# Optimization experiments

Hardware: AMD Instinct MI355X
Metric: run time of the kernel (lower is better)

The kernel has to match this reference:

```python
import jax, jax.numpy as jnp
import numpy as np
from jax.scipy.special import i0

# --- module constants (from Transform.__init__) ---
H = 320          # image size per dim
OS = 2           # grid oversampling ratio
G = H * OS       # oversampled grid size (640)
W = 6            # Kaiser-Bessel kernel width (torchkbnufft default numpoints)
BETA = float(np.pi * np.sqrt((W / OS) ** 2 * (OS - 0.5) ** 2 - 0.8))  # Beatty beta
S_FULL = 800     # spokes in full trajectory
R = H * OS       # readout points per spoke (640)
B, C = 8, 1      # slices, coils


def _golden_traj(n_spokes, n_read):
    """Golden-angle radial trajectory; k radius = H/2 = 160 (matches traj/160*pi scaling)."""
    ga = np.pi * 2.0 / (1.0 + np.sqrt(5.0))  # ~111.246 degrees
    ang = np.arange(n_spokes) * ga
    r = np.linspace(-H / 2, H / 2, n_read, endpoint=False)
    kx = (r[None, :] * np.cos(ang)[:, None]).astype(np.float32)
    ky = (r[None, :] * np.sin(ang)[:, None]).astype(np.float32)
    return kx, ky


def _kb(d):
    """Kaiser-Bessel kernel, d in oversampled-grid units, support |d|<=W/2."""
    arg = jnp.clip(1.0 - (2.0 * d / W) ** 2, 0.0, None)
    return i0(BETA * jnp.sqrt(arg)) / i0(jnp.float32(BETA))


def _apod1d(n):
    """Analytic Fourier transform of the KB kernel -> image-domain apodization."""
    f = (jnp.arange(n, dtype=jnp.float32) - n / 2) / G  # cycles per grid sample
    t = BETA ** 2 - (jnp.pi * W * f) ** 2
    z = jnp.maximum(jnp.sqrt(jnp.abs(t)), 1e-7)
    a = jnp.where(t > 0, jnp.sinh(z), jnp.sin(z)) / z
    return a / a[n // 2]  # normalize center to 1


def _ktoi(k):
    """Centered inverse 2D FFT (k-space -> image)."""
    return jnp.fft.fftshift(
        jnp.fft.ifft2(jnp.fft.ifftshift(k, axes=(-2, -1)), axes=(-2, -1), norm='ortho'),
        axes=(-2, -1))


def _mean_std_norm_complex(x):
    ax = (-3, -2, -1)
    def n(v):
        m = v.mean(axis=ax, keepdims=True)
        s = v.std(axis=ax, keepdims=True, ddof=1)  # torch std default: unbiased
        return (v - m) / s
    return n(x.real) + 1j * n(x.imag)


def _nufft(image, traj_kx, traj_ky):
    """Type-2 KB NUFFT: image (B,C,H,H) complex -> k samples (B,C,S,R)."""
    S, Rr = traj_kx.shape
    # apodization correction then oversampled centered FFT
    ap = _apod1d(H)
    x = image / (ap[:, None] * ap[None, :])
    xp = jnp.zeros(image.shape[:-2] + (G, G), jnp.complex64)
    xp = xp.at[..., H // 2:H // 2 + H, H // 2:H // 2 + H].set(x)
    Xos = jnp.fft.fft2(jnp.fft.ifftshift(xp, axes=(-2, -1)), axes=(-2, -1))
    # non-uniform grid coords: omega = traj/160*pi -> g = omega*G/(2pi) = traj*G/H
    gx = (traj_kx * (G / H)).reshape(-1)  # (P,)
    gy = (traj_ky * (G / H)).reshape(-1)
    ix0 = jnp.floor(gx).astype(jnp.int32) - W // 2 + 1
    iy0 = jnp.floor(gy).astype(jnp.int32) - W // 2 + 1
    out = jnp.zeros(image.shape[:-2] + (gx.shape[0],), jnp.complex64)
    for jx in range(W):  # fixed 6x6 neighbor taps
        ixu = ix0 + jx
        wx = _kb(gx - ixu)
        ix = jnp.mod(ixu, G)
        for jy in range(W):
            iyu = iy0 + jy
            w = (wx * _kb(gy - iyu)).astype(jnp.complex64)
            iy = jnp.mod(iyu, G)
            out = out + w * Xos[..., ix, iy]
    return out.reshape(image.shape[:-2] + (S, Rr))


def setup_inputs() -> dict:
    key = jax.random.key(0)
    k1, k2 = jax.random.split(key)
    kspace_r = jax.random.normal(k1, (B, C, H, H), jnp.float32)
    kspace_i = jax.random.normal(k2, (B, C, H, H), jnp.float32)
    tkx, tky = _golden_traj(S_FULL, R)
    return {'kspace_r': kspace_r, 'kspace_i': kspace_i,
            'traj_kx': jnp.asarray(tkx), 'traj_ky': jnp.asarray(tky)}


def reference(kspace_r, kspace_i, traj_kx, traj_ky):
    kspace = (kspace_r + 1j * kspace_i).astype(jnp.complex64)
    image = _mean_std_norm_complex(_ktoi(kspace))
    kspace_full = _nufft(image, traj_kx, traj_ky)
    return kspace_full
```

## Files before the change

kernel.cpp:

```cpp
#include <hip/hip_runtime.h>
#include <math.h>

#ifndef M_PI
#define M_PI 3.14159265358979323846
#endif

#define HH   320
#define GG   640
#define NB   8
#define PTS  512000

typedef __attribute__((ext_vector_type(8))) short short8_t;
typedef __attribute__((ext_vector_type(4))) float f32x4;

__device__ __forceinline__ float bessel_i0f(float x){
  if (x < 3.75f){
    float t = (x*x) * (1.0f/(3.75f*3.75f));
    return 1.0f + t*(3.5156229f + t*(3.0899424f + t*(1.2067492f +
                 t*(0.2659732f + t*(0.0360768f + t*0.0045813f)))));
  } else {
    float t = 3.75f/x;
    float p = 0.39894228f + t*(0.01328592f + t*(0.00225319f + t*(-0.00157565f +
              t*(0.00916281f + t*(-0.02057706f + t*(0.02635537f +
              t*(-0.01647633f + t*0.00392377f)))))));
    return expf(x)*rsqrtf(x)*p;
  }
}

__device__ __forceinline__ float kbw(float d, float beta, float inv_i0b){
  float q = d * 0.33333333333333f;
  float u = 1.0f - q*q;
  u = fmaxf(u, 0.0f);
  return bessel_i0f(beta * sqrtf(u)) * inv_i0b;
}

__device__ __forceinline__ short bfr(float x){
  unsigned u = __float_as_uint(x);
  u = (u + 0x7fffu + ((u>>16)&1u)) >> 16;
  return (short)u;
}
__device__ __forceinline__ unsigned pkbf(float2 v){
  unsigned a = __float_as_uint(v.x);
  a = (a + 0x7fffu + ((a>>16)&1u)) >> 16;
  unsigned b = __float_as_uint(v.y);
  b = (b + 0x7fffu + ((b>>16)&1u)) & 0xffff0000u;
  return a | b;
}

__global__ void build_m1bf(short* __restrict__ M1r, short* __restrict__ M1i){
  int idx = blockIdx.x*256 + threadIdx.x;
  if (idx >= HH*HH) return;
  int x = idx / HH, k = idx - x*HH;
  int r = (x*k) % HH;
  float ang = (float)r * (6.283185307179586f/(float)HH);
  float s, c; sincosf(ang, &s, &c);
  float sg = ((x + k) & 1) ? -0.05590169943749474f : 0.05590169943749474f;
  M1r[idx] = bfr(sg*c);
  M1i[idx] = bfr(sg*s);
}

__global__ void build_w2(short* __restrict__ Wr, short* __restrict__ Wi){
  int idx = blockIdx.x*256 + threadIdx.x;
  if (idx >= GG*HH) return;
  int k = idx / HH, m = idx - k*HH;
  int t = (k * (m - 160)) % GG; if (t < 0) t += GG;
  float ang = (float)t * (6.283185307179586f/(float)GG);
  float s, c; sincosf(ang, &s, &c);
  Wr[idx] = bfr(c);
  Wi[idx] = bfr(-s);
}

__global__ void build_rap(float* __restrict__ rap, float beta){
  int n = threadIdx.x;
  if (n >= HH) return;
  float f = (float)(n - 160) * (1.0f/(float)GG);
  float w = 3.14159265358979f * 6.0f * f;
  float t = beta*beta - w*w;
  float z = fmaxf(sqrtf(fabsf(t)), 1e-7f);
  float a = (t > 0.0f ? sinhf(z) : sinf(z)) / z;
  float a0 = sinhf(beta) / beta;
  rap[n] = a0 / a;
}

__global__ void pack_bf(const float* __restrict__ re, const float* __restrict__ im,
                        short* __restrict__ Kr, short* __restrict__ Ki, int n){
  int i = blockIdx.x*256 + threadIdx.x;
  if (i < n){ Kr[i] = bfr(re[i]); Ki[i] = bfr(im[i]); }
}

__global__ __launch_bounds__(512)
void gemm1_mfma(const short* __restrict__ M1r, const short* __restrict__ M1i,
                const short* __restrict__ Kr,  const short* __restrict__ Ki,
                short* __restrict__ Ttr, short* __restrict__ Tti)
{
  int nwg = gridDim.x, orig = blockIdx.x;
  int qn = nwg>>3, rn = nwg&7;
  int xcd = orig&7, pos = orig>>3;
  int wg = (xcd<rn ? xcd*(qn+1) : rn*(qn+1)+(xcd-rn)*qn) + pos;
  int ti = wg % 20, tj = wg / 20;
  int i0 = ti*16, j0 = tj*16;
  int l = threadIdx.x & 63, wid = threadIdx.x >> 6;

  long aoff = (long)(j0 + (l&15))*HH + ((l>>4)<<3);
  const short* pmr = M1r + aoff;
  const short* pmi = M1i + aoff;
  long boff = (long)wid*102400 + (long)(i0 + (l&15))*HH + ((l>>4)<<3);
  const short* pkr = Kr + boff;
  const short* pki = Ki + boff;

  f32x4 accRa = {0.f,0.f,0.f,0.f}, accRb = {0.f,0.f,0.f,0.f}, accI = {0.f,0.f,0.f,0.f};
  #pragma unroll
  for (int kt = 0; kt < 320; kt += 32){
    short8_t mR = *(const short8_t*)(pmr + kt);
    short8_t mI = *(const short8_t*)(pmi + kt);
    short8_t kR = *(const short8_t*)(pkr + kt);
    short8_t kI = *(const short8_t*)(pki + kt);
    accRa = __builtin_amdgcn_mfma_f32_16x16x32_bf16(mR, kR, accRa, 0,0,0);
    accRb = __builtin_amdgcn_mfma_f32_16x16x32_bf16(mI, kI, accRb, 0,0,0);
    accI  = __builtin_amdgcn_mfma_f32_16x16x32_bf16(mR, kI, accI, 0,0,0);
    accI  = __builtin_amdgcn_mfma_f32_16x16x32_bf16(mI, kR, accI, 0,0,0);
  }
  int col = l & 15, r0 = (l>>4)*4;
  #pragma unroll
  for (int r=0;r<4;r++){
    long o = (long)wid*102400 + (long)(j0+r0+r)*HH + i0+col;
    Ttr[o] = bfr(accRa[r] - accRb[r]);
    Tti[o] = bfr(accI[r]);
  }
}

__global__ __launch_bounds__(512)
void gemm2_mfma(const short* __restrict__ M1r, const short* __restrict__ M1i,
                const short* __restrict__ Ttr, const short* __restrict__ Tti,
                float2* __restrict__ P)
{
  int nwg = gridDim.x, orig = blockIdx.x;
  int qn = nwg>>3, rn = nwg&7;
  int xcd = orig&7, pos = orig>>3;
  int wg = (xcd<rn ? xcd*(qn+1) : rn*(qn+1)+(xcd-rn)*qn) + pos;
  int tj = wg % 20, ti = wg / 20;
  int i0 = ti*16, j0 = tj*16;
  int l = threadIdx.x & 63, wid = threadIdx.x >> 6;

  long aoff = (long)(i0 + (l&15))*HH + ((l>>4)<<3);
  const short* pmr = M1r + aoff;
  const short* pmi = M1i + aoff;
  long boff = (long)wid*102400 + (long)(j0 + (l&15))*HH + ((l>>4)<<3);
  const short* ptr = Ttr + boff;
  const short* pti = Tti + boff;

  f32x4 accRa = {0.f,0.f,0.f,0.f}, accRb = {0.f,0.f,0.f,0.f}, accI = {0.f,0.f,0.f,0.f};
  #pragma unroll
  for (int kt = 0; kt < 320; kt += 32){
    short8_t mR = *(const short8_t*)(pmr + kt);
    short8_t mI = *(const short8_t*)(pmi + kt);
    short8_t tR = *(const short8_t*)(ptr + kt);
    short8_t tI = *(const short8_t*)(pti + kt);
    accRa = __builtin_amdgcn_mfma_f32_16x16x32_bf16(mR, tR, accRa, 0,0,0);
    accRb = __builtin_amdgcn_mfma_f32_16x16x32_bf16(mI, tI, accRb, 0,0,0);
    accI  = __builtin_amdgcn_mfma_f32_16x16x32_bf16(mR, tI, accI, 0,0,0);
    accI  = __builtin_amdgcn_mfma_f32_16x16x32_bf16(mI, tR, accI, 0,0,0);
  }
  int col = l & 15, r0 = (l>>4)*4;
  #pragma unroll
  for (int r=0;r<4;r++){
    long o = (long)wid*102400 + (long)(i0+r0+r)*HH + j0+col;
    P[o] = make_float2(accRa[r] - accRb[r], accI[r]);
  }
}

__global__ void stats_part(const float2* __restrict__ img, double* __restrict__ part){
  int slice = blockIdx.y, seg = blockIdx.x;
  const float2* p = img + (long)slice*(HH*HH) + (long)seg*3200;
  double sr=0.0, si=0.0, srr=0.0, sii=0.0;
  for (int i = threadIdx.x; i < 3200; i += 256){
    float2 v = p[i];
    sr += (double)v.x; si += (double)v.y;
    srr += (double)v.x*(double)v.x; sii += (double)v.y*(double)v.y;
  }
  __shared__ double sh[256];
  double vals[4] = {sr, si, srr, sii};
  #pragma unroll
  for (int q=0;q<4;q++){
    sh[threadIdx.x] = vals[q];
    __syncthreads();
    for (int s=128; s>0; s>>=1){
      if (threadIdx.x < s) sh[threadIdx.x] += sh[threadIdx.x + s];
      __syncthreads();
    }
    if (threadIdx.x == 0) part[((long)slice*32 + seg)*4 + q] = sh[0];
    __syncthreads();
  }
}

__global__ void stats_fin(const double* __restrict__ part, float4* __restrict__ stats){
  int b = blockIdx.x;
  int t = threadIdx.x;
  __shared__ double sh[64];
  double red[4];
  #pragma unroll
  for (int q=0;q<4;q++){
    sh[t] = (t < 32) ? part[((long)b*32 + t)*4 + q] : 0.0;
    __syncthreads();
    for (int s=32; s>0; s>>=1){
      if (t < s) sh[t] += sh[t + s];
      __syncthreads();
    }
    red[q] = sh[0];
    __syncthreads();
  }
  if (t == 0){
    double N = (double)(HH*HH);
    double mr = red[0]/N, mi = red[1]/N;
    double vr = (red[2] - N*mr*mr)/(N-1.0);
    double vi = (red[3] - N*mi*mi)/(N-1.0);
    stats[b] = make_float4((float)mr, (float)mi,
                           (float)(1.0/sqrt(vr)), (float)(1.0/sqrt(vi)));
  }
}

__global__ __launch_bounds__(256)
void tnorm(const float2* __restrict__ img, const float4* __restrict__ stats,
           const float* __restrict__ rap,
           short* __restrict__ xnTr, short* __restrict__ xnTi){
  __shared__ float2 tile[32][33];
  int b = blockIdx.z;
  int i0 = blockIdx.y*32, j0 = blockIdx.x*32;
  int tx = threadIdx.x & 31, ty = threadIdx.x >> 5;
  float4 st = stats[b];
  #pragma unroll
  for (int r=0;r<4;r++){
    int i = i0 + ty + r*8, j = j0 + tx;
    float2 v = img[(long)b*102400 + (long)i*HH + j];
    float sc = rap[i]*rap[j];
    tile[ty+r*8][tx] = make_float2((v.x-st.x)*st.z*sc, (v.y-st.y)*st.w*sc);
  }
  __syncthreads();
  #pragma unroll
  for (int r=0;r<4;r++){
    int j = j0 + ty + r*8, i = i0 + tx;
    float2 v = tile[tx][ty+r*8];
    long o = (long)b*102400 + (long)j*HH + i;
    xnTr[o] = bfr(v.x);
    xnTi[o] = bfr(v.y);
  }
}

template<int NC>
__global__ __launch_bounds__(64*NC)
void cgemm3_mfma(const short* __restrict__ Wr, const short* __restrict__ Wi,
                 const short* __restrict__ xnTr, const short* __restrict__ xnTi,
                 short* __restrict__ Ur, short* __restrict__ Ui, int slice0)
{
  int nwg = gridDim.x, orig = blockIdx.x;
  int qn = nwg>>3, rn = nwg&7;
  int xcd = orig&7, pos = orig>>3;
  int wg = (xcd<rn ? xcd*(qn+1) : rn*(qn+1)+(xcd-rn)*qn) + pos;
  int bj = wg % 20, bi = wg / 20;
  int i0 = bi*16, j0 = bj*16;
  int l = threadIdx.x & 63, wid = threadIdx.x >> 6;

  long aoff = (long)(i0 + (l&15))*HH + ((l>>4)<<3);
  const short* pwr = Wr + aoff;
  const short* pwi = Wi + aoff;
  long boff = (long)(slice0+wid)*102400 + (long)(j0 + (l&15))*HH + ((l>>4)<<3);
  const short* pxr = xnTr + boff;
  const short* pxi = xnTi + boff;

  f32x4 accRa = {0.f,0.f,0.f,0.f}, accRb = {0.f,0.f,0.f,0.f}, accI = {0.f,0.f,0.f,0.f};
  #pragma unroll
  for (int kt = 0; kt < 320; kt += 32){
    short8_t wR = *(const short8_t*)(pwr + kt);
    short8_t wI = *(const short8_t*)(pwi + kt);
    short8_t xR = *(const short8_t*)(pxr + kt);
    short8_t xI = *(const short8_t*)(pxi + kt);
    accRa = __builtin_amdgcn_mfma_f32_16x16x32_bf16(wR, xR, accRa, 0,0,0);
    accRb = __builtin_amdgcn_mfma_f32_16x16x32_bf16(wI, xI, accRb, 0,0,0);
    accI  = __builtin_amdgcn_mfma_f32_16x16x32_bf16(wR, xI, accI, 0,0,0);
    accI  = __builtin_amdgcn_mfma_f32_16x16x32_bf16(wI, xR, accI, 0,0,0);
  }
  int col = l & 15, r0 = (l>>4)*4;
  #pragma unroll
  for (int r=0;r<4;r++){
    long o = (long)wid*204800 + (long)(i0+r0+r)*HH + j0+col;
    Ur[o] = bfr(accRa[r] - accRb[r]);
    Ui[o] = bfr(accI[r]);
  }
}

template<int NC>
__global__ __launch_bounds__(64*NC)
void cgemm4_mfma(const short* __restrict__ Ur, const short* __restrict__ Ui,
                 const short* __restrict__ Wr, const short* __restrict__ Wi,
                 unsigned* __restrict__ Xos)
{
  __shared__ unsigned sh[256*NC];
  int nwg = gridDim.x, orig = blockIdx.x;
  int qn = nwg>>3, rn = nwg&7;
  int xcd = orig&7, pos = orig>>3;
  int wg = (xcd<rn ? xcd*(qn+1) : rn*(qn+1)+(xcd-rn)*qn) + pos;
  int bj = wg % 40, bi = wg / 40;
  int i0 = bi*16, j0 = bj*16;
  int l = threadIdx.x & 63, wid = threadIdx.x >> 6;

  long aoff = (long)wid*204800 + (long)(i0 + (l&15))*HH + ((l>>4)<<3);
  const short* par = Ur + aoff;
  const short* pai = Ui + aoff;
  long boff = (long)(j0 + (l&15))*HH + ((l>>4)<<3);
  const short* pbr = Wr + boff;
  const short* pbi = Wi + boff;

  f32x4 accRa = {0.f,0.f,0.f,0.f}, accRb = {0.f,0.f,0.f,0.f}, accI = {0.f,0.f,0.f,0.f};
  #pragma unroll
  for (int kt = 0; kt < 320; kt += 32){
    short8_t aR = *(const short8_t*)(par + kt);
    short8_t aI = *(const short8_t*)(pai + kt);
    short8_t bR = *(const short8_t*)(pbr + kt);
    short8_t bI = *(const short8_t*)(pbi + kt);
    accRa = __builtin_amdgcn_mfma_f32_16x16x32_bf16(aR, bR, accRa, 0,0,0);
    accRb = __builtin_amdgcn_mfma_f32_16x16x32_bf16(aI, bI, accRb, 0,0,0);
    accI  = __builtin_amdgcn_mfma_f32_16x16x32_bf16(aR, bI, accI, 0,0,0);
    accI  = __builtin_amdgcn_mfma_f32_16x16x32_bf16(aI, bR, accI, 0,0,0);
  }

  int col = l & 15, r0 = (l>>4)*4;
  #pragma unroll
  for (int r=0;r<4;r++)
    sh[(r0+r)*16*NC + col*NC + wid] = pkbf(make_float2(accRa[r]-accRb[r], accI[r]));
  __syncthreads();

  int t = threadIdx.x;
  int row = t/(4*NC), q = t - row*(4*NC);
  uint4 v = ((const uint4*)(sh + row*16*NC))[q];
  ((uint4*)(Xos + ((long)(i0+row)*GG + j0)*NC))[q] = v;
}

template<int NC>
__global__ __launch_bounds__(384)
void interp6(const float* __restrict__ tkx, const float* __restrict__ tky,
             const unsigned* __restrict__ Xos, float* __restrict__ out,
             int slice0, int cplx, float beta, float inv_i0b){
  __shared__ float2 sh[NC][6][64];
  __shared__ float swy[6][64];
  int tid = threadIdx.x;
  int ptl = tid & 63;
  int jx  = tid >> 6;
  int p   = blockIdx.x*64 + ptl;

  float gx = tkx[p]*2.0f, gy = tky[p]*2.0f;
  int ix0 = (int)floorf(gx) - 2;
  int iy0 = (int)floorf(gy) - 2;

  int ixu = ix0 + jx;
  int ixm = (ixu < 0) ? ixu + GG : ((ixu >= GG) ? ixu - GG : ixu);
  float wxj = kbw(gx - (float)ixu, beta, inv_i0b);
  swy[jx][ptl] = kbw(gy - (float)(iy0 + jx), beta, inv_i0b);

  int iym[6];
  #pragma unroll
  for (int j=0;j<6;j++){
    int iyu = iy0 + j;
    iym[j] = (iyu < 0) ? iyu + GG : ((iyu >= GG) ? iyu - GG : iyu);
  }
  __syncthreads();
  float wy[6];
  #pragma unroll
  for (int j=0;j<6;j++) wy[j] = swy[j][ptl];

  float2 acc[NC];
  #pragma unroll
  for (int s=0;s<NC;s++) acc[s] = make_float2(0.f, 0.f);

  const unsigned* rowp = Xos + (long)ixm*(GG*NC);
  #pragma unroll
  for (int jy=0;jy<6;jy++){
    float w = wy[jy];
    const unsigned* s2 = rowp + iym[jy]*NC;
    unsigned uu[NC];
    if constexpr (NC == 8){
      uint4 v0 = ((const uint4*)s2)[0], v1 = ((const uint4*)s2)[1];
      uu[0]=v0.x; uu[1]=v0.y; uu[2]=v0.z; uu[3]=v0.w;
      uu[4]=v1.x; uu[5]=v1.y; uu[6]=v1.z; uu[7]=v1.w;
    } else if constexpr (NC == 4){
      uint4 v = *(const uint4*)s2;
      uu[0]=v.x; uu[1]=v.y; uu[2]=v.z; uu[3]=v.w;
    } else if constexpr (NC == 2){
      uint2 v = *(const uint2*)s2;
      uu[0]=v.x; uu[1]=v.y;
    } else {
      uu[0] = s2[0];
    }
    #pragma unroll
    for (int s=0;s<NC;s++){
      float re = __uint_as_float(uu[s] << 16);
      float im = __uint_as_float(uu[s] & 0xffff0000u);
      acc[s].x = fmaf(w, re, acc[s].x);
      acc[s].y = fmaf(w, im, acc[s].y);
    }
  }
  #pragma unroll
  for (int s=0;s<NC;s++)
    sh[s][jx][ptl] = make_float2(acc[s].x*wxj, acc[s].y*wxj);
  __syncthreads();

  for (int t2 = tid; t2 < 64*NC; t2 += 384){
    int pt = t2 & 63;
    int s  = t2 >> 6;
    float2 r = make_float2(0.f, 0.f);
    #pragma unroll
    for (int j=0;j<6;j++){
      float2 v = sh[s][j][pt];
      r.x += v.x; r.y += v.y;
    }
    long pg = (long)blockIdx.x*64 + pt;
    if (cplx){
      ((float2*)out)[(long)(slice0+s)*PTS + pg] = r;
    } else {
      out[(long)(slice0+s)*PTS + pg] = r.x;
    }
  }
}

extern "C" void kernel_launch(void* const* d_in, const int* in_sizes, int n_in,
                              void* d_out, int out_size, void* d_ws, size_t ws_size,
                              hipStream_t stream) {
  const float* kr  = (const float*)d_in[0];
  const float* ki  = (const float*)d_in[1];
  const float* tkx = (const float*)d_in[2];
  const float* tky = (const float*)d_in[3];
  char* ws = (char*)d_ws;

  short*  M1r   = (short*)(ws + 0);
  short*  M1i   = (short*)(ws + 204800);
  short*  Wr    = (short*)(ws + 409600);
  short*  Wi    = (short*)(ws + 819200);
  float*  rap   = (float*) (ws + 1228800);
  float4* stats = (float4*)(ws + 1230080);
  double* part  = (double*)(ws + 1230208);
  short*  Kr    = (short*)(ws + 1238400);
  short*  Ki    = (short*)(ws + 2876800);
  short*  Ttr   = (short*)(ws + 4515200);
  short*  Tti   = (short*)(ws + 6153600);
  float2* P     = (float2*)(ws + 7792000);
  short*  xnTr  = (short*)(ws + 14345600);
  short*  xnTi  = (short*)(ws + 15984000);

  int nc = 1;
  if      (ws_size >= (size_t)(17622400 + 8L*1638400)) nc = 8;
  else if (ws_size >= (size_t)(17622400 + 4L*1638400)) nc = 4;
  else if (ws_size >= (size_t)(17622400 + 2L*1638400)) nc = 2;
  if (ws_size < (size_t)(17622400 + 1638400)) return;

  short*    Ur  = (short*)(ws + 7792000);
  short*    Ui  = (short*)(ws + 7792000 + (long)nc*409600);
  unsigned* Xos = (unsigned*)(ws + 17622400);

  int cplx = (out_size >= 8192000) ? 1 : 0;

  double beta_d = M_PI * sqrt(9.0*2.25 - 0.8);
  double qq = beta_d*beta_d/4.0, term = 1.0, i0b = 1.0;
  for (int k=1;k<64;k++){ term *= qq/((double)k*(double)k); i0b += term; }
  float beta = (float)beta_d;
  float inv_i0b = (float)(1.0/i0b);

  build_m1bf<<<400, 256, 0, stream>>>(M1r, M1i);
  build_w2  <<<800, 256, 0, stream>>>(Wr, Wi);
  build_rap <<<1,   320, 0, stream>>>(rap, beta);
  pack_bf   <<<3200,256, 0, stream>>>(kr, ki, Kr, Ki, NB*HH*HH);

  gemm1_mfma<<<400, 512, 0, stream>>>(M1r, M1i, Kr, Ki, Ttr, Tti);
  gemm2_mfma<<<400, 512, 0, stream>>>(M1r, M1i, Ttr, Tti, P);
  stats_part<<<dim3(32,NB), 256, 0, stream>>>(P, part);
  stats_fin <<<NB, 64, 0, stream>>>(part, stats);
  tnorm<<<dim3(10,10,NB), 256, 0, stream>>>(P, stats, rap, xnTr, xnTi);

  for (int c = 0; c < NB/nc; ++c){
    switch (nc){
      case 8:
        cgemm3_mfma<8><<<800, 512,0,stream>>>(Wr,Wi,xnTr,xnTi,Ur,Ui, c*8);
        cgemm4_mfma<8><<<1600,512,0,stream>>>(Ur,Ui,Wr,Wi,Xos);
        interp6<8><<<8000,384,0,stream>>>(tkx,tky,Xos,(float*)d_out, c*8, cplx, beta, inv_i0b);
        break;
      case 4:
        cgemm3_mfma<4><<<800, 256,0,stream>>>(Wr,Wi,xnTr,xnTi,Ur,Ui, c*4);
        cgemm4_mfma<4><<<1600,256,0,stream>>>(Ur,Ui,Wr,Wi,Xos);
        interp6<4><<<8000,384,0,stream>>>(tkx,tky,Xos,(float*)d_out, c*4, cplx, beta, inv_i0b);
        break;
      case 2:
        cgemm3_mfma<2><<<800, 128,0,stream>>>(Wr,Wi,xnTr,xnTi,Ur,Ui, c*2);
        cgemm4_mfma<2><<<1600,128,0,stream>>>(Ur,Ui,Wr,Wi,Xos);
        interp6<2><<<8000,384,0,stream>>>(tkx,tky,Xos,(float*)d_out, c*2, cplx, beta, inv_i0b);
        break;
      default:
        cgemm3_mfma<1><<<800,  64,0,stream>>>(Wr,Wi,xnTr,xnTi,Ur,Ui, c);
        cgemm4_mfma<1><<<1600, 64,0,stream>>>(Ur,Ui,Wr,Wi,Xos);
        interp6<1><<<8000,384,0,stream>>>(tkx,tky,Xos,(float*)d_out, c, cplx, beta, inv_i0b);
        break;
    }
  }
}
```

Before: 299.4 us.

## Fuse setup kernels, fold stats into gemm2, store bf16 image, use 32x32 MFMA

Merges the four setup kernels into one launch. The mean/variance statistics are now reduced inside gemm2's epilogue with wavefront shuffles, which removes the stats_part pass. The intermediate image is stored as bf16 planes instead of float2, halving that traffic. The cgemm3/cgemm4 stages switch from 16x16x32 to 32x32x16 MFMA tiles with four times fewer workgroups, trading parallelism for more reuse per instruction. The bf16 image adds rounding before normalization, and the statistics are now accumulated in float per lane before the double reduction.

```diff
diff --git a/kernel.cpp b/kernel.cpp
--- a/kernel.cpp
+++ b/kernel.cpp
@@ -10,8 +10,9 @@
 #define NB   8
 #define PTS  512000
 
-typedef __attribute__((ext_vector_type(8))) short short8_t;
-typedef __attribute__((ext_vector_type(4))) float f32x4;
+typedef __attribute__((ext_vector_type(8)))  short short8_t;
+typedef __attribute__((ext_vector_type(4)))  float f32x4;
+typedef __attribute__((ext_vector_type(16))) float f32x16;
 
 __device__ __forceinline__ float bessel_i0f(float x){
   if (x < 3.75f){
@@ -39,6 +40,9 @@
   u = (u + 0x7fffu + ((u>>16)&1u)) >> 16;
   return (short)u;
 }
+__device__ __forceinline__ float bf2f(short v){
+  return __uint_as_float(((unsigned)(unsigned short)v) << 16);
+}
 __device__ __forceinline__ unsigned pkbf(float2 v){
   unsigned a = __float_as_uint(v.x);
   a = (a + 0x7fffu + ((a>>16)&1u)) >> 16;
@@ -47,45 +51,48 @@
   return a | b;
 }
 
-__global__ void build_m1bf(short* __restrict__ M1r, short* __restrict__ M1i){
-  int idx = blockIdx.x*256 + threadIdx.x;
-  if (idx >= HH*HH) return;
-  int x = idx / HH, k = idx - x*HH;
-  int r = (x*k) % HH;
-  float ang = (float)r * (6.283185307179586f/(float)HH);
-  float s, c; sincosf(ang, &s, &c);
-  float sg = ((x + k) & 1) ? -0.05590169943749474f : 0.05590169943749474f;
-  M1r[idx] = bfr(sg*c);
-  M1i[idx] = bfr(sg*s);
-}
-
-__global__ void build_w2(short* __restrict__ Wr, short* __restrict__ Wi){
-  int idx = blockIdx.x*256 + threadIdx.x;
-  if (idx >= GG*HH) return;
-  int k = idx / HH, m = idx - k*HH;
-  int t = (k * (m - 160)) % GG; if (t < 0) t += GG;
-  float ang = (float)t * (6.283185307179586f/(float)GG);
-  float s, c; sincosf(ang, &s, &c);
-  Wr[idx] = bfr(c);
-  Wi[idx] = bfr(-s);
-}
-
-__global__ void build_rap(float* __restrict__ rap, float beta){
-  int n = threadIdx.x;
-  if (n >= HH) return;
-  float f = (float)(n - 160) * (1.0f/(float)GG);
-  float w = 3.14159265358979f * 6.0f * f;
-  float t = beta*beta - w*w;
-  float z = fmaxf(sqrtf(fabsf(t)), 1e-7f);
-  float a = (t > 0.0f ? sinhf(z) : sinf(z)) / z;
-  float a0 = sinhf(beta) / beta;
-  rap[n] = a0 / a;
-}
-
-__global__ void pack_bf(const float* __restrict__ re, const float* __restrict__ im,
-                        short* __restrict__ Kr, short* __restrict__ Ki, int n){
-  int i = blockIdx.x*256 + threadIdx.x;
-  if (i < n){ Kr[i] = bfr(re[i]); Ki[i] = bfr(im[i]); }
+__global__ void build_all(const float* __restrict__ kr, const float* __restrict__ ki,
+                          short* __restrict__ M1r, short* __restrict__ M1i,
+                          short* __restrict__ Wr,  short* __restrict__ Wi,
+                          float* __restrict__ rap,
+                          short* __restrict__ Kr,  short* __restrict__ Ki,
+                          float beta){
+  int blk = blockIdx.x, tid = threadIdx.x;
+  if (blk < 400){
+    int idx = blk*256 + tid;
+    if (idx >= HH*HH) return;
+    int x = idx / HH, k = idx - x*HH;
+    int r = (x*k) % HH;
+    float ang = (float)r * (6.283185307179586f/(float)HH);
+    float s, c; sincosf(ang, &s, &c);
+    float sg = ((x + k) & 1) ? -0.05590169943749474f : 0.05590169943749474f;
+    M1r[idx] = bfr(sg*c);
+    M1i[idx] = bfr(sg*s);
+  } else if (blk < 1200){
+    int idx = (blk-400)*256 + tid;
+    if (idx >= GG*HH) return;
+    int k = idx / HH, m = idx - k*HH;
+    int t = (k * (m - 160)) % GG; if (t < 0) t += GG;
+    float ang = (float)t * (6.283185307179586f/(float)GG);
+    float s, c; sincosf(ang, &s, &c);
+    Wr[idx] = bfr(c);
+    Wi[idx] = bfr(-s);
+  } else if (blk < 4400){
+    int idx = (blk-1200)*256 + tid;
+    if (idx >= NB*HH*HH) return;
+    Kr[idx] = bfr(kr[idx]);
+    Ki[idx] = bfr(ki[idx]);
+  } else {
+    for (int n = tid; n < HH; n += 256){
+      float f = (float)(n - 160) * (1.0f/(float)GG);
+      float w = 3.14159265358979f * 6.0f * f;
+      float t = beta*beta - w*w;
+      float z = fmaxf(sqrtf(fabsf(t)), 1e-7f);
+      float a = (t > 0.0f ? sinhf(z) : sinf(z)) / z;
+      float a0 = sinhf(beta) / beta;
+      rap[n] = a0 / a;
+    }
+  }
 }
 
 __global__ __launch_bounds__(512)
@@ -132,7 +139,8 @@
 __global__ __launch_bounds__(512)
 void gemm2_mfma(const short* __restrict__ M1r, const short* __restrict__ M1i,
                 const short* __restrict__ Ttr, const short* __restrict__ Tti,
-                float2* __restrict__ P)
+                short* __restrict__ Pr, short* __restrict__ Pi,
+                double* __restrict__ part)
 {
   int nwg = gridDim.x, orig = blockIdx.x;
   int qn = nwg>>3, rn = nwg&7;
@@ -162,47 +170,48 @@
     accI  = __builtin_amdgcn_mfma_f32_16x16x32_bf16(mI, tR, accI, 0,0,0);
   }
   int col = l & 15, r0 = (l>>4)*4;
+  float sr=0.f, si=0.f, srr=0.f, sii=0.f;
   #pragma unroll
   for (int r=0;r<4;r++){
+    float re = accRa[r] - accRb[r];
+    float im = accI[r];
     long o = (long)wid*102400 + (long)(i0+r0+r)*HH + j0+col;
-    P[o] = make_float2(accRa[r] - accRb[r], accI[r]);
-  }
-}
-
-__global__ void stats_part(const float2* __restrict__ img, double* __restrict__ part){
-  int slice = blockIdx.y, seg = blockIdx.x;
-  const float2* p = img + (long)slice*(HH*HH) + (long)seg*3200;
-  double sr=0.0, si=0.0, srr=0.0, sii=0.0;
-  for (int i = threadIdx.x; i < 3200; i += 256){
-    float2 v = p[i];
-    sr += (double)v.x; si += (double)v.y;
-    srr += (double)v.x*(double)v.x; sii += (double)v.y*(double)v.y;
-  }
-  __shared__ double sh[256];
-  double vals[4] = {sr, si, srr, sii};
-  #pragma unroll
-  for (int q=0;q<4;q++){
-    sh[threadIdx.x] = vals[q];
-    __syncthreads();
-    for (int s=128; s>0; s>>=1){
-      if (threadIdx.x < s) sh[threadIdx.x] += sh[threadIdx.x + s];
-      __syncthreads();
-    }
-    if (threadIdx.x == 0) part[((long)slice*32 + seg)*4 + q] = sh[0];
-    __syncthreads();
+    Pr[o] = bfr(re);
+    Pi[o] = bfr(im);
+    sr += re; si += im; srr += re*re; sii += im*im;
+  }
+  double d0 = sr, d1 = si, d2 = srr, d3 = sii;
+  #pragma unroll
+  for (int off = 32; off > 0; off >>= 1){
+    d0 += __shfl_down(d0, off);
+    d1 += __shfl_down(d1, off);
+    d2 += __shfl_down(d2, off);
+    d3 += __shfl_down(d3, off);
+  }
+  if (l == 0){
+    long pidx = ((long)wid*400 + wg)*4;
+    part[pidx  ] = d0;
+    part[pidx+1] = d1;
+    part[pidx+2] = d2;
+    part[pidx+3] = d3;
   }
 }
 
 __global__ void stats_fin(const double* __restrict__ part, float4* __restrict__ stats){
   int b = blockIdx.x;
   int t = threadIdx.x;
-  __shared__ double sh[64];
+  __shared__ double sh[256];
+  double loc[4] = {0.0,0.0,0.0,0.0};
+  for (int w = t; w < 400; w += 256){
+    const double* p = part + ((long)b*400 + w)*4;
+    loc[0] += p[0]; loc[1] += p[1]; loc[2] += p[2]; loc[3] += p[3];
+  }
   double red[4];
   #pragma unroll
   for (int q=0;q<4;q++){
-    sh[t] = (t < 32) ? part[((long)b*32 + t)*4 + q] : 0.0;
+    sh[t] = loc[q];
     __syncthreads();
-    for (int s=32; s>0; s>>=1){
+    for (int s=128; s>0; s>>=1){
       if (t < s) sh[t] += sh[t + s];
       __syncthreads();
     }
@@ -220,8 +229,8 @@
 }
 
 __global__ __launch_bounds__(256)
-void tnorm(const float2* __restrict__ img, const float4* __restrict__ stats,
-           const float* __restrict__ rap,
+void tnorm(const short* __restrict__ Pr, const short* __restrict__ Pi,
+           const float4* __restrict__ stats, const float* __restrict__ rap,
            short* __restrict__ xnTr, short* __restrict__ xnTi){
   __shared__ float2 tile[32][33];
   int b = blockIdx.z;
@@ -231,9 +240,10 @@
   #pragma unroll
   for (int r=0;r<4;r++){
     int i = i0 + ty + r*8, j = j0 + tx;
-    float2 v = img[(long)b*102400 + (long)i*HH + j];
+    long o = (long)b*102400 + (long)i*HH + j;
+    float re = bf2f(Pr[o]), im = bf2f(Pi[o]);
     float sc = rap[i]*rap[j];
-    tile[ty+r*8][tx] = make_float2((v.x-st.x)*st.z*sc, (v.y-st.y)*st.w*sc);
+    tile[ty+r*8][tx] = make_float2((re-st.x)*st.z*sc, (im-st.y)*st.w*sc);
   }
   __syncthreads();
   #pragma unroll
@@ -256,33 +266,34 @@
   int qn = nwg>>3, rn = nwg&7;
   int xcd = orig&7, pos = orig>>3;
   int wg = (xcd<rn ? xcd*(qn+1) : rn*(qn+1)+(xcd-rn)*qn) + pos;
-  int bj = wg % 20, bi = wg / 20;
-  int i0 = bi*16, j0 = bj*16;
+  int bj = wg % 10, bi = wg / 10;
+  int i0 = bi*32, j0 = bj*32;
   int l = threadIdx.x & 63, wid = threadIdx.x >> 6;
 
-  long aoff = (long)(i0 + (l&15))*HH + ((l>>4)<<3);
+  long aoff = (long)(i0 + (l&31))*HH + ((l>>5)<<3);
   const short* pwr = Wr + aoff;
   const short* pwi = Wi + aoff;
-  long boff = (long)(slice0+wid)*102400 + (long)(j0 + (l&15))*HH + ((l>>4)<<3);
+  long boff = (long)(slice0+wid)*102400 + (long)(j0 + (l&31))*HH + ((l>>5)<<3);
   const short* pxr = xnTr + boff;
   const short* pxi = xnTi + boff;
 
-  f32x4 accRa = {0.f,0.f,0.f,0.f}, accRb = {0.f,0.f,0.f,0.f}, accI = {0.f,0.f,0.f,0.f};
-  #pragma unroll
-  for (int kt = 0; kt < 320; kt += 32){
+  f32x16 accRa = {0.f}, accRb = {0.f}, accI = {0.f};
+  #pragma unroll
+  for (int kt = 0; kt < 320; kt += 16){
     short8_t wR = *(const short8_t*)(pwr + kt);
     short8_t wI = *(const short8_t*)(pwi + kt);
     short8_t xR = *(const short8_t*)(pxr + kt);
     short8_t xI = *(const short8_t*)(pxi + kt);
-    accRa = __builtin_amdgcn_mfma_f32_16x16x32_bf16(wR, xR, accRa, 0,0,0);
-    accRb = __builtin_amdgcn_mfma_f32_16x16x32_bf16(wI, xI, accRb, 0,0,0);
-    accI  = __builtin_amdgcn_mfma_f32_16x16x32_bf16(wR, xI, accI, 0,0,0);
-    accI  = __builtin_amdgcn_mfma_f32_16x16x32_bf16(wI, xR, accI, 0,0,0);
-  }
-  int col = l & 15, r0 = (l>>4)*4;
-  #pragma unroll
-  for (int r=0;r<4;r++){
-    long o = (long)wid*204800 + (long)(i0+r0+r)*HH + j0+col;
+    accRa = __builtin_amdgcn_mfma_f32_32x32x16_bf16(wR, xR, accRa, 0,0,0);
+    accRb = __builtin_amdgcn_mfma_f32_32x32x16_bf16(wI, xI, accRb, 0,0,0);
+    accI  = __builtin_amdgcn_mfma_f32_32x32x16_bf16(wR, xI, accI, 0,0,0);
+    accI  = __builtin_amdgcn_mfma_f32_32x32x16_bf16(wI, xR, accI, 0,0,0);
+  }
+  int col = l & 31, rhi = 4*(l>>5);
+  #pragma unroll
+  for (int r=0;r<16;r++){
+    int row = (r&3) + 8*(r>>2) + rhi;
+    long o = (long)wid*204800 + (long)(i0+row)*HH + j0+col;
     Ur[o] = bfr(accRa[r] - accRb[r]);
     Ui[o] = bfr(accI[r]);
   }
@@ -294,45 +305,52 @@
                  const short* __restrict__ Wr, const short* __restrict__ Wi,
                  unsigned* __restrict__ Xos)
 {
-  __shared__ unsigned sh[256*NC];
+  __shared__ unsigned sh[1024*NC];
   int nwg = gridDim.x, orig = blockIdx.x;
   int qn = nwg>>3, rn = nwg&7;
   int xcd = orig&7, pos = orig>>3;
   int wg = (xcd<rn ? xcd*(qn+1) : rn*(qn+1)+(xcd-rn)*qn) + pos;
-  int bj = wg % 40, bi = wg / 40;
-  int i0 = bi*16, j0 = bj*16;
+  int bj = wg % 20, bi = wg / 20;
+  int i0 = bi*32, j0 = bj*32;
   int l = threadIdx.x & 63, wid = threadIdx.x >> 6;
 
-  long aoff = (long)wid*204800 + (long)(i0 + (l&15))*HH + ((l>>4)<<3);
+  long aoff = (long)wid*204800 + (long)(i0 + (l&31))*HH + ((l>>5)<<3);
   const short* par = Ur + aoff;
   const short* pai = Ui + aoff;
-  long boff = (long)(j0 + (l&15))*HH + ((l>>4)<<3);
+  long boff = (long)(j0 + (l&31))*HH + ((l>>5)<<3);
   const short* pbr = Wr + boff;
   const short* pbi = Wi + boff;
 
-  f32x4 accRa = {0.f,0.f,0.f,0.f}, accRb = {0.f,0.f,0.f,0.f}, accI = {0.f,0.f,0.f,0.f};
-  #pragma unroll
-  for (int kt = 0; kt < 320; kt += 32){
+  f32x16 accRa = {0.f}, accRb = {0.f}, accI = {0.f};
+  #pragma unroll
+  for (int kt = 0; kt < 320; kt += 16){
     short8_t aR = *(const short8_t*)(par + kt);
     short8_t aI = *(const short8_t*)(pai + kt);
     short8_t bR = *(const short8_t*)(pbr + kt);
     short8_t bI = *(const short8_t*)(pbi + kt);
-    accRa = __builtin_amdgcn_mfma_f32_16x16x32_bf16(aR, bR, accRa, 0,0,0);
-    accRb = __builtin_amdgcn_mfma_f32_16x16x32_bf16(aI, bI, accRb, 0,0,0);
-    accI  = __builtin_amdgcn_mfma_f32_16x16x32_bf16(aR, bI, accI, 0,0,0);
-    accI  = __builtin_amdgcn_mfma_f32_16x16x32_bf16(aI, bR, accI, 0,0,0);
-  }
-
-  int col = l & 15, r0 = (l>>4)*4;
-  #pragma unroll
-  for (int r=0;r<4;r++)
-    sh[(r0+r)*16*NC + col*NC + wid] = pkbf(make_float2(accRa[r]-accRb[r], accI[r]));
+    accRa = __builtin_amdgcn_mfma_f32_32x32x16_bf16(aR, bR, accRa, 0,0,0);
+    accRb = __builtin_amdgcn_mfma_f32_32x32x16_bf16(aI, bI, accRb, 0,0,0);
+    accI  = __builtin_amdgcn_mfma_f32_32x32x16_bf16(aR, bI, accI, 0,0,0);
+    accI  = __builtin_amdgcn_mfma_f32_32x32x16_bf16(aI, bR, accI, 0,0,0);
+  }
+
+  int col = l & 31, rhi = 4*(l>>5);
+  #pragma unroll
+  for (int r=0;r<16;r++){
+    int row = (r&3) + 8*(r>>2) + rhi;
+    sh[row*32*NC + col*NC + wid] = pkbf(make_float2(accRa[r]-accRb[r], accI[r]));
+  }
   __syncthreads();
 
-  int t = threadIdx.x;
-  int row = t/(4*NC), q = t - row*(4*NC);
-  uint4 v = ((const uint4*)(sh + row*16*NC))[q];
-  ((uint4*)(Xos + ((long)(i0+row)*GG + j0)*NC))[q] = v;
+  int tid = threadIdx.x;
+  #pragma unroll
+  for (int q=0;q<4;q++){
+    int idx = tid + 64*NC*q;
+    int row = idx / (8*NC);
+    int w   = idx - row*(8*NC);
+    uint4 v = ((const uint4*)(sh + row*32*NC))[w];
+    ((uint4*)(Xos + ((long)(i0+row)*GG + j0)*NC))[w] = v;
+  }
 }
 
 template<int NC>
@@ -437,23 +455,24 @@
   float*  rap   = (float*) (ws + 1228800);
   float4* stats = (float4*)(ws + 1230080);
   double* part  = (double*)(ws + 1230208);
-  short*  Kr    = (short*)(ws + 1238400);
-  short*  Ki    = (short*)(ws + 2876800);
-  short*  Ttr   = (short*)(ws + 4515200);
-  short*  Tti   = (short*)(ws + 6153600);
-  float2* P     = (float2*)(ws + 7792000);
-  short*  xnTr  = (short*)(ws + 14345600);
-  short*  xnTi  = (short*)(ws + 15984000);
+  short*  Kr    = (short*)(ws + 1332608);
+  short*  Ki    = (short*)(ws + 2971008);
+  short*  Ttr   = (short*)(ws + 4609408);
+  short*  Tti   = (short*)(ws + 6247808);
+  short*  Pr    = (short*)(ws + 7886208);
+  short*  Pi    = (short*)(ws + 9524608);
+  short*  xnTr  = (short*)(ws + 11163008);
+  short*  xnTi  = (short*)(ws + 12801408);
 
   int nc = 1;
-  if      (ws_size >= (size_t)(17622400 + 8L*1638400)) nc = 8;
-  else if (ws_size >= (size_t)(17622400 + 4L*1638400)) nc = 4;
-  else if (ws_size >= (size_t)(17622400 + 2L*1638400)) nc = 2;
-  if (ws_size < (size_t)(17622400 + 1638400)) return;
-
-  short*    Ur  = (short*)(ws + 7792000);
-  short*    Ui  = (short*)(ws + 7792000 + (long)nc*409600);
-  unsigned* Xos = (unsigned*)(ws + 17622400);
+  if      (ws_size >= (size_t)(14439808 + 8L*1638400)) nc = 8;
+  else if (ws_size >= (size_t)(14439808 + 4L*1638400)) nc = 4;
+  else if (ws_size >= (size_t)(14439808 + 2L*1638400)) nc = 2;
+  if (ws_size < (size_t)(14439808 + 1638400)) return;
+
+  short*    Ur  = (short*)(ws + 1332608);
+  short*    Ui  = (short*)(ws + 1332608 + (long)nc*409600);
+  unsigned* Xos = (unsigned*)(ws + 14439808);
 
   int cplx = (out_size >= 8192000) ? 1 : 0;
 
@@ -463,37 +482,33 @@
   float beta = (float)beta_d;
   float inv_i0b = (float)(1.0/i0b);
 
-  build_m1bf<<<400, 256, 0, stream>>>(M1r, M1i);
-  build_w2  <<<800, 256, 0, stream>>>(Wr, Wi);
-  build_rap <<<1,   320, 0, stream>>>(rap, beta);
-  pack_bf   <<<3200,256, 0, stream>>>(kr, ki, Kr, Ki, NB*HH*HH);
+  build_all<<<4401, 256, 0, stream>>>(kr, ki, M1r, M1i, Wr, Wi, rap, Kr, Ki, beta);
 
   gemm1_mfma<<<400, 512, 0, stream>>>(M1r, M1i, Kr, Ki, Ttr, Tti);
-  gemm2_mfma<<<400, 512, 0, stream>>>(M1r, M1i, Ttr, Tti, P);
-  stats_part<<<dim3(32,NB), 256, 0, stream>>>(P, part);
-  stats_fin <<<NB, 64, 0, stream>>>(part, stats);
-  tnorm<<<dim3(10,10,NB), 256, 0, stream>>>(P, stats, rap, xnTr, xnTi);
+  gemm2_mfma<<<400, 512, 0, stream>>>(M1r, M1i, Ttr, Tti, Pr, Pi, part);
+  stats_fin <<<NB, 256, 0, stream>>>(part, stats);
+  tnorm<<<dim3(10,10,NB), 256, 0, stream>>>(Pr, Pi, stats, rap, xnTr, xnTi);
 
   for (int c = 0; c < NB/nc; ++c){
     switch (nc){
       case 8:
-        cgemm3_mfma<8><<<800, 512,0,stream>>>(Wr,Wi,xnTr,xnTi,Ur,Ui, c*8);
-        cgemm4_mfma<8><<<1600,512,0,stream>>>(Ur,Ui,Wr,Wi,Xos);
+        cgemm3_mfma<8><<<200, 512,0,stream>>>(Wr,Wi,xnTr,xnTi,Ur,Ui, c*8);
+        cgemm4_mfma<8><<<400, 512,0,stream>>>(Ur,Ui,Wr,Wi,Xos);
         interp6<8><<<8000,384,0,stream>>>(tkx,tky,Xos,(float*)d_out, c*8, cplx, beta, inv_i0b);
         break;
       case 4:
-        cgemm3_mfma<4><<<800, 256,0,stream>>>(Wr,Wi,xnTr,xnTi,Ur,Ui, c*4);
-        cgemm4_mfma<4><<<1600,256,0,stream>>>(Ur,Ui,Wr,Wi,Xos);
+        cgemm3_mfma<4><<<200, 256,0,stream>>>(Wr,Wi,xnTr,xnTi,Ur,Ui, c*4);
+        cgemm4_mfma<4><<<400, 256,0,stream>>>(Ur,Ui,Wr,Wi,Xos);
         interp6<4><<<8000,384,0,stream>>>(tkx,tky,Xos,(float*)d_out, c*4, cplx, beta, inv_i0b);
         break;
       case 2:
-        cgemm3_mfma<2><<<800, 128,0,stream>>>(Wr,Wi,xnTr,xnTi,Ur,Ui, c*2);
-        cgemm4_mfma<2><<<1600,128,0,stream>>>(Ur,Ui,Wr,Wi,Xos);
+        cgemm3_mfma<2><<<200, 128,0,stream>>>(Wr,Wi,xnTr,xnTi,Ur,Ui, c*2);
+        cgemm4_mfma<2><<<400, 128,0,stream>>>(Ur,Ui,Wr,Wi,Xos);
         interp6<2><<<8000,384,0,stream>>>(tkx,tky,Xos,(float*)d_out, c*2, cplx, beta, inv_i0b);
         break;
       default:
-        cgemm3_mfma<1><<<800,  64,0,stream>>>(Wr,Wi,xnTr,xnTi,Ur,Ui, c);
-        cgemm4_mfma<1><<<1600, 64,0,stream>>>(Ur,Ui,Wr,Wi,Xos);
+        cgemm3_mfma<1><<<200,  64,0,stream>>>(Wr,Wi,xnTr,xnTi,Ur,Ui, c);
+        cgemm4_mfma<1><<<400,  64,0,stream>>>(Ur,Ui,Wr,Wi,Xos);
         interp6<1><<<8000,384,0,stream>>>(tkx,tky,Xos,(float*)d_out, c, cplx, beta, inv_i0b);
         break;
     }
```

Measured after the change: 248.3 us. -17.1%, faster.
